# Optimization experiments

Measured on AMD Instinct MI355X. Metric: run time of the kernel, lower is better.

The kernel has to match this reference:

```python
import jax, jax.numpy as jnp
import numpy as np

V, D, M = 13000, 300, 500   # vocab, embed dim, cell/mem size (hardcoded in source)
B, NW, T = 64, 5, 128       # episodes, ways, seq len
EPS = 1e-8                  # torch cosine_similarity default eps


def setup_inputs():
    key = jax.random.key(0)
    ks = jax.random.split(key, 14)
    s = 0.05  # xavier-ish scale
    return {
        "support_tokens": jax.random.randint(ks[0], (B, NW, T), 0, V, dtype=jnp.int32),
        "target_tokens": jax.random.randint(ks[1], (B, T), 0, V, dtype=jnp.int32),
        "blank_pos_support": jax.random.randint(ks[2], (B, NW), 0, T, dtype=jnp.int32),
        "blank_pos_target": jax.random.randint(ks[3], (B,), 0, T, dtype=jnp.int32),
        "target_y": jax.random.randint(ks[4], (B,), 0, NW, dtype=jnp.int32),
        "emb": jax.random.normal(ks[5], (V, D)) * s,
        "WL": jax.random.normal(ks[6], (3, M, D)) * s,
        "UL": jax.random.normal(ks[7], (3, M, M)) * s,
        "bL": jnp.zeros((3, M)),
        "WR": jax.random.normal(ks[8], (3, M, D)) * s,
        "UR": jax.random.normal(ks[9], (3, M, M)) * s,
        "bR": jnp.zeros((3, M)),
        "Wo": jax.random.normal(ks[10], (D, M)) * s,
        "Uo": jax.random.normal(ks[11], (D, M)) * s,
        "bo": jnp.zeros((D,)),
        "c0L": jnp.zeros((M,)),
        "c0R": jnp.zeros((M,)),
    }


def _cell_scan(x, W, U, b, c0):
    # x: [T, D] -> pre-update cell states (the 'env' the source appends BEFORE updating _c): [T, M]
    gx = jnp.einsum('td,gmd->tgm', x, W) + b  # input projections for all 3 gates, all timesteps
    def step(c, g):
        g = g + jnp.einsum('gmh,h->gm', U, c)
        f = jax.nn.sigmoid(g[0])
        i = jax.nn.sigmoid(g[1])
        cbar = jnp.tanh(g[2])
        return f * c + i * cbar, c
    _, pre = jax.lax.scan(step, c0, gx)
    return pre


def _blank_env(tokens, blank_pos, emb, WL, UL, bL, WR, UR, bR, Wo, Uo, bo, c0L, c0R):
    # tokens: [N, T], blank_pos: [N] -> env vector at blank position: [N, D]
    x = emb[tokens]  # [N, T, D]
    Lenv = jax.vmap(lambda xs: _cell_scan(xs, WL, UL, bL, c0L))(x)          # [N, T, M]
    Renv = jax.vmap(lambda xs: _cell_scan(xs[::-1], WR, UR, bR, c0R))(x)[:, ::-1]
    n = jnp.arange(tokens.shape[0])
    l = Lenv[n, blank_pos]  # [N, M]
    r = Renv[n, blank_pos]  # source pairs Lenv[i] with Renv[T-1-i] of the reversed list == right pre-state at pos i
    return jnp.tanh(l @ Wo.T + r @ Uo.T + bo)  # oNN: unbatched_Linear(lev=0, tanh)


def reference(support_tokens, target_tokens, blank_pos_support, blank_pos_target,
              target_y, emb, WL, UL, bL, WR, UR, bR, Wo, Uo, bo, c0L, c0R):
    b, nw, t = support_tokens.shape
    sup = _blank_env(support_tokens.reshape(b * nw, t), blank_pos_support.reshape(b * nw),
                     emb, WL, UL, bL, WR, UR, bR, Wo, Uo, bo, c0L, c0R).reshape(b, nw, -1)
    tgt = _blank_env(target_tokens, blank_pos_target,
                     emb, WL, UL, bL, WR, UR, bR, Wo, Uo, bo, c0L, c0R)  # [B, D]
    # cosine similarity per way, scaled by 10 (fce LSTM output is discarded in the source, so omitted)
    dot = jnp.einsum('bnd,bd->bn', sup, tgt)
    denom = jnp.maximum(jnp.linalg.norm(sup, axis=-1) * jnp.linalg.norm(tgt, axis=-1)[:, None], EPS)
    z = (dot / denom) * 10.0  # [B, NW]
    probs = jax.nn.softmax(z, axis=1)
    accuracy = jnp.mean((jnp.argmax(probs, axis=1) == target_y).astype(jnp.float32))
    # F.cross_entropy applied to the softmax probs (double softmax), as in the source
    logp = jax.nn.log_softmax(probs, axis=1)
    loss = -jnp.mean(jnp.take_along_axis(logp, target_y[:, None].astype(jnp.int32), axis=1))
    return accuracy, loss
```

## Files before the change

### kernel.cpp

```cpp
#include <hip/hip_runtime.h>
#include <math.h>

#define V 13000
#define D 300
#define M 500
#define B 64
#define NW 5
#define T 128
#define NSUP (B*NW)
#define NSEQ (NSUP + B)
#define CT 32
#define NCT 12
#define MT 16
#define KSPL 4
#define CHK 20
#define CKS 10
#define KROW 800
#define NSTEP (T-1)
#define ASTR 68
#define BSTR 36
#define APW (CHK*ASTR)
#define BPW (CHK*BSTR)
#define SMSZ (KSPL*(APW+BPW))
#define NCOMP 768
#define NGATH 12

__device__ __forceinline__ float sigmoidf_(float x){ return 1.0f/(1.0f+expf(-x)); }


__global__ void init_kernel(const float* __restrict__ c0L, const float* __restrict__ c0R,
                            float* __restrict__ actB0, float* __restrict__ c_final)
{
    int idx = blockIdx.x*256 + threadIdx.x;
    if (idx >= 2*M*NSEQ) return;
    int d = idx / (M*NSEQ);
    int rem = idx % (M*NSEQ);
    int m = rem / NSEQ;
    int r = rem % NSEQ;
    float v = d ? c0R[m] : c0L[m];
    actB0[((size_t)d*KROW + 300 + m)*NSEQ + r] = v;
    c_final[((size_t)d*NSEQ + r)*M + m] = v;
}

__global__ void sort_kernel(const int* __restrict__ blank_sup, const int* __restrict__ blank_tgt,
                            int* __restrict__ perm, int* __restrict__ lenR, int* __restrict__ tmax)
{
    __shared__ int L0[NSEQ], L1[NSEQ];
    int tid = threadIdx.x;
    int blank = (tid < NSUP) ? blank_sup[tid] : blank_tgt[tid - NSUP];
    int l0 = blank, l1 = (T-1) - blank;
    L0[tid] = l0; L1[tid] = l1;
    __syncthreads();
    int r0 = 0, r1 = 0;
    for (int j = 0; j < NSEQ; ++j) {
        int c = L0[j]; r0 += (c > l0) || (c == l0 && j < tid);
        int d = L1[j]; r1 += (d > l1) || (d == l1 && j < tid);
    }
    perm[r0] = tid;        lenR[r0] = l0;
    perm[NSEQ + r1] = tid; lenR[NSEQ + r1] = l1;
    __syncthreads();
    if (tid < 2*NCT) {
        int dir = tid / NCT, t = tid % NCT;
        tmax[tid] = lenR[dir*NSEQ + t*CT];
    }
}

__global__ __launch_bounds__(256)
void step_kernel(int s,
                 const float* __restrict__ actB_cur, float* __restrict__ actB_next,
                 float* __restrict__ c_final,
                 const float* __restrict__ WL, const float* __restrict__ UL, const float* __restrict__ bL,
                 const float* __restrict__ WR, const float* __restrict__ UR, const float* __restrict__ bR,
                 const int* __restrict__ perm, const int* __restrict__ lenR, const int* __restrict__ tmax,
                 const int* __restrict__ sup_tok, const int* __restrict__ tgt_tok,
                 const float* __restrict__ emb)
{
    const int bid = blockIdx.x;
    const int tid = threadIdx.x;

    if (bid >= NCOMP) {
        const int gb = bid - NCOMP;
        const int d  = gb / 6;
        const int rt = gb % 6;
        const int sn = s + 1;
        if (sn >= NSTEP) return;
        if (sn >= tmax[d*NCT + 2*rt]) return;
        const int rr = tid & 63;
        const int kk = tid >> 6;
        const int rank = rt*64 + rr;
        const int ch = perm[d*NSEQ + rank];
        const int tpos = d ? (T-1 - sn) : sn;
        const int tok = (ch < NSUP) ? sup_tok[ch*T + tpos] : tgt_tok[(ch-NSUP)*T + tpos];
        const float* src = emb + (size_t)tok*D + kk;
        float* dst = actB_next + (size_t)d*KROW*NSEQ + rank;
        #pragma unroll 5
        for (int k4 = 0; k4 < 75; ++k4) {
            dst[(size_t)(k4*4 + kk)*NSEQ] = src[k4*4];
        }
        return;
    }
    if (s < 0) return;

    const int ct = bid >> 6;
    const int dm = bid & 63;
    const int d  = dm >> 5;
    const int mt = dm & 31;
    if (s >= tmax[d*NCT + ct]) return;

    __shared__ float smem[SMSZ];

    const int ks   = tid >> 6;
    const int lane = tid & 63;
    const int ty   = lane >> 3;
    const int tx   = lane & 7;
    const int rank0 = ct*CT;

    const float* Wd = d ? WR : WL;
    const float* Ud = d ? UR : UL;
    const float* bias = d ? bR : bL;

    float* As = smem + ks*APW;
    float* Bs = smem + KSPL*APW + ks*BPW;

    const float* aW[4]; const float* aU[4]; float* aD[4];
    #pragma unroll
    for (int i = 0; i < 4; ++i) {
        int slot = lane + 64*i; if (slot >= 240) slot = 239;
        int row = slot/5, kq = slot%5;
        int g = row >> 4, ml = row & 15;
        int m = mt*MT + ml; if (m >= M) m = M-1;
        aW[i] = Wd + (size_t)(g*M + m)*D + kq*4;
        aU[i] = Ud + (size_t)(g*M + m)*M + kq*4;
        aD[i] = As + kq*4*ASTR + ml*4 + g;
    }
    const bool a3 = (lane < 48);
    const float* bS[3]; float* bD[3];
    #pragma unroll
    for (int i = 0; i < 3; ++i) {
        int slot = lane + 64*i; if (slot >= 160) slot = 159;
        int kk = slot >> 3, c4 = slot & 7;
        bS[i] = actB_cur + ((size_t)d*KROW + kk)*NSEQ + rank0 + c4*4;
        bD[i] = Bs + kk*BSTR + c4*4;
    }
    const bool b2 = (lane < 32);

    float4 aR4[4]; float4 bR4[3];
    auto loadA = [&](int gc){
        const int off = (gc < 15) ? gc*CHK : gc*CHK - 300;
        const bool isx = (gc < 15);
        aR4[0] = *(const float4*)((isx ? aW[0] : aU[0]) + off);
        aR4[1] = *(const float4*)((isx ? aW[1] : aU[1]) + off);
        aR4[2] = *(const float4*)((isx ? aW[2] : aU[2]) + off);
        if (a3) aR4[3] = *(const float4*)((isx ? aW[3] : aU[3]) + off);
    };
    auto loadB = [&](int gc){
        const size_t ofs = (size_t)(gc*CHK)*NSEQ;
        bR4[0] = *(const float4*)(bS[0] + ofs);
        bR4[1] = *(const float4*)(bS[1] + ofs);
        if (b2) bR4[2] = *(const float4*)(bS[2] + ofs);
    };
    auto writeAB = [&](){
        #pragma unroll
        for (int i = 0; i < 4; ++i) {
            if (i == 3 && !a3) break;
            float* p = aD[i];
            p[0] = aR4[i].x; p[ASTR] = aR4[i].y; p[2*ASTR] = aR4[i].z; p[3*ASTR] = aR4[i].w;
        }
        *(float4*)bD[0] = bR4[0];
        *(float4*)bD[1] = bR4[1];
        if (b2) *(float4*)bD[2] = bR4[2];
    };

    float4 acc[2][3];
    #pragma unroll
    for (int j=0;j<2;++j)
        #pragma unroll
        for (int g=0;g<3;++g) acc[j][g] = make_float4(0.f,0.f,0.f,0.f);

    const float* Ard = As + ty*8;
    const float* Brd = Bs + tx*4;

#define FMA4(AC, AV, BV) AC.x += (AV)*(BV).x; AC.y += (AV)*(BV).y; AC.z += (AV)*(BV).z; AC.w += (AV)*(BV).w;

    loadA(ks*CKS); loadB(ks*CKS);
    for (int ck = 0; ck < CKS; ++ck) {
        writeAB();
        if (ck + 1 < CKS) { loadA(ks*CKS + ck + 1); loadB(ks*CKS + ck + 1); }
        #pragma unroll
        for (int kk = 0; kk < CHK; ++kk) {
            float4 a0 = *(const float4*)(Ard + kk*ASTR);
            float4 a1 = *(const float4*)(Ard + kk*ASTR + 4);
            float4 b  = *(const float4*)(Brd + kk*BSTR);
            FMA4(acc[0][0], a0.x, b);
            FMA4(acc[0][1], a0.y, b);
            FMA4(acc[0][2], a0.z, b);
            FMA4(acc[1][0], a1.x, b);
            FMA4(acc[1][1], a1.y, b);
            FMA4(acc[1][2], a1.z, b);
        }
    }
#undef FMA4

    __syncthreads();
    float* red = smem;
    #pragma unroll
    for (int j=0;j<2;++j) {
        int ml = ty*2 + j;
        #pragma unroll
        for (int g=0;g<3;++g)
            *(float4*)&red[((ks*MT + ml)*3 + g)*CT + tx*4] = acc[j][g];
    }
    __syncthreads();

    #pragma unroll
    for (int q=0;q<2;++q) {
        int cell = tid*2 + q;
        int ml = cell >> 5, c = cell & 31;
        int m = mt*MT + ml;
        if (m < M) {
            float g0 = bias[m], g1 = bias[M + m], g2 = bias[2*M + m];
            #pragma unroll
            for (int kq=0;kq<KSPL;++kq) {
                g0 += red[((kq*MT + ml)*3 + 0)*CT + c];
                g1 += red[((kq*MT + ml)*3 + 1)*CT + c];
                g2 += red[((kq*MT + ml)*3 + 2)*CT + c];
            }
            int rank = rank0 + c;
            int len  = lenR[d*NSEQ + rank];
            size_t cidx = ((size_t)d*KROW + 300 + m)*NSEQ + rank;
            float cold = actB_cur[cidx];
            float f  = sigmoidf_(g0);
            float i2 = sigmoidf_(g1);
            float cb = tanhf(g2);
            float cn = (s < len) ? (f*cold + i2*cb) : cold;
            actB_next[cidx] = cn;
            if (s == len - 1) {
                int ch = perm[d*NSEQ + rank];
                c_final[((size_t)d*NSEQ + ch)*M + m] = cn;
            }
        }
    }
}

__global__ void env_kernel(const float* __restrict__ l_states, const float* __restrict__ r_states,
                           const float* __restrict__ Wo, const float* __restrict__ Uo,
                           const float* __restrict__ bo,
                           float* __restrict__ env)
{
    __shared__ __align__(16) float l[M];
    __shared__ __align__(16) float r[M];
    const int i = blockIdx.x;
    const int tid = threadIdx.x;
    for (int m=tid; m<M; m+=blockDim.x){ l[m]=l_states[i*M+m]; r[m]=r_states[i*M+m]; }
    __syncthreads();
    for (int d=tid; d<D; d+=blockDim.x) {
        const float4* wo = reinterpret_cast<const float4*>(Wo + (size_t)d*M);
        const float4* uo = reinterpret_cast<const float4*>(Uo + (size_t)d*M);
        const float4* lv = reinterpret_cast<const float4*>(l);
        const float4* rv = reinterpret_cast<const float4*>(r);
        float acc = bo[d];
        #pragma unroll 5
        for (int q=0; q<M/4; ++q) {
            float4 a=wo[q], bv=lv[q], u=uo[q], rr=rv[q];
            acc += a.x*bv.x + a.y*bv.y + a.z*bv.z + a.w*bv.w;
            acc += u.x*rr.x + u.y*rr.y + u.z*rr.z + u.w*rr.w;
        }
        env[i*D + d] = tanhf(acc);
    }
}

__global__ void episode_kernel(const float* __restrict__ env, const int* __restrict__ target_y,
                               float* __restrict__ flags, float* __restrict__ losses)
{
    const int b = blockIdx.x;
    const int lane = threadIdx.x;
    const float* tgt = env + (size_t)(NSUP + b)*D;

    float tn = 0.f;
    for (int d=lane; d<D; d+=64){ float v=tgt[d]; tn += v*v; }
    for (int off=32; off; off>>=1) tn += __shfl_down(tn, off);
    tn = __shfl(tn, 0);

    float z[NW];
    for (int n=0; n<NW; ++n){
        const float* sup = env + (size_t)(b*NW + n)*D;
        float dot=0.f, sn=0.f;
        for (int d=lane; d<D; d+=64){ float sv=sup[d], tv=tgt[d]; dot+=sv*tv; sn+=sv*sv; }
        for (int off=32; off; off>>=1){ dot += __shfl_down(dot,off); sn += __shfl_down(sn,off); }
        dot = __shfl(dot,0); sn = __shfl(sn,0);
        float denom = fmaxf(sqrtf(sn)*sqrtf(tn), 1e-8f);
        z[n] = dot/denom*10.0f;
    }

    if (lane==0){
        float mx=z[0];
        for(int n=1;n<NW;n++) mx=fmaxf(mx,z[n]);
        float se=0.f; float p[NW];
        for(int n=0;n<NW;n++){ p[n]=expf(z[n]-mx); se+=p[n]; }
        for(int n=0;n<NW;n++) p[n]/=se;
        int am=0; float bv=p[0];
        for(int n=1;n<NW;n++) if(p[n]>bv){bv=p[n];am=n;}
        int y = target_y[b];
        flags[b] = (am==y)?1.0f:0.0f;
        float mx2=p[0]; for(int n=1;n<NW;n++) mx2=fmaxf(mx2,p[n]);
        float se2=0.f; for(int n=0;n<NW;n++) se2+=expf(p[n]-mx2);
        losses[b] = -(p[y]-mx2-logf(se2));
    }
}

__global__ void finalize_kernel(const float* __restrict__ flags, const float* __restrict__ losses,
                                float* __restrict__ out)
{
    const int lane = threadIdx.x;
    float f = flags[lane], l = losses[lane];
    for (int off=32; off; off>>=1){ f += __shfl_down(f,off); l += __shfl_down(l,off); }
    if (lane==0){ out[0] = f/(float)B; out[1] = l/(float)B; }
}

extern "C" void kernel_launch(void* const* d_in, const int* in_sizes, int n_in,
                              void* d_out, int out_size, void* d_ws, size_t ws_size,
                              hipStream_t stream) {
    const int*   sup_tok   = (const int*)d_in[0];
    const int*   tgt_tok   = (const int*)d_in[1];
    const int*   blank_sup = (const int*)d_in[2];
    const int*   blank_tgt = (const int*)d_in[3];
    const int*   target_y  = (const int*)d_in[4];
    const float* emb = (const float*)d_in[5];
    const float* WL  = (const float*)d_in[6];
    const float* UL  = (const float*)d_in[7];
    const float* bL  = (const float*)d_in[8];
    const float* WR  = (const float*)d_in[9];
    const float* UR  = (const float*)d_in[10];
    const float* bR  = (const float*)d_in[11];
    const float* Wo  = (const float*)d_in[12];
    const float* Uo  = (const float*)d_in[13];
    const float* bo  = (const float*)d_in[14];
    const float* c0L = (const float*)d_in[15];
    const float* c0R = (const float*)d_in[16];

    const size_t ACTSZ = (size_t)2*KROW*NSEQ;
    float* ws_f = (float*)d_ws;
    float* actB0   = ws_f;
    float* actB1   = actB0 + ACTSZ;
    float* c_final = actB1 + ACTSZ;
    float* env     = c_final + 2*NSEQ*M;
    float* flags   = env + NSEQ*D;
    float* losses  = flags + B;
    int*   perm    = (int*)(losses + B);
    int*   lenR    = perm + 2*NSEQ;
    int*   tmax    = lenR + 2*NSEQ;

    init_kernel<<<(2*M*NSEQ + 255)/256, 256, 0, stream>>>(c0L, c0R, actB0, c_final);
    sort_kernel<<<1, NSEQ, 0, stream>>>(blank_sup, blank_tgt, perm, lenR, tmax);

    step_kernel<<<NCOMP + NGATH, 256, 0, stream>>>(-1, actB1, actB0, c_final,
                                                   WL, UL, bL, WR, UR, bR,
                                                   perm, lenR, tmax, sup_tok, tgt_tok, emb);
    for (int s = 0; s < NSTEP; ++s) {
        float* cur  = (s & 1) ? actB1 : actB0;
        float* next = (s & 1) ? actB0 : actB1;
        step_kernel<<<NCOMP + NGATH, 256, 0, stream>>>(s, cur, next, c_final,
                                                       WL, UL, bL, WR, UR, bR,
                                                       perm, lenR, tmax, sup_tok, tgt_tok, emb);
    }

    env_kernel<<<NSEQ, 256, 0, stream>>>(c_final, c_final + NSEQ*M, Wo, Uo, bo, env);
    episode_kernel<<<B, 64, 0, stream>>>(env, target_y, flags, losses);
    finalize_kernel<<<1, 64, 0, stream>>>(flags, losses, (float*)d_out);
}
```

Baseline: 5.100 ms.

## Stream activations from global into registers, keep only weights in LDS

The per-step gate GEMM no longer stages the activation tile through shared memory. Each thread now computes one m-row by three gates by eight columns, reading activation rows straight from global memory through a four-deep register prefetch ring. Only weight rows are written to LDS, in a row-major layout with float4 stores, and the LDS footprint shrinks to what the reduction needs; a launch-bounds occupancy hint of 3 is added. This removes the activation LDS writes and reads, but the 16 lanes sharing a column group now issue duplicate global loads, which depend on L1 broadcast.

```diff
diff --git a/kernel.cpp b/kernel.cpp
--- a/kernel.cpp
+++ b/kernel.cpp
@@ -17,11 +17,9 @@
 #define CKS 10
 #define KROW 800
 #define NSTEP (T-1)
-#define ASTR 68
-#define BSTR 36
-#define APW (CHK*ASTR)
-#define BPW (CHK*BSTR)
-#define SMSZ (KSPL*(APW+BPW))
+#define ASTR 28
+#define APW (48*ASTR)
+#define SMSZ 6144
 #define NCOMP 768
 #define NGATH 12
 
@@ -65,7 +63,7 @@
     }
 }
 
-__global__ __launch_bounds__(256)
+__global__ __launch_bounds__(256, 3)
 void step_kernel(int s,
                  const float* __restrict__ actB_cur, float* __restrict__ actB_next,
                  float* __restrict__ c_final,
@@ -94,9 +92,8 @@
         const float* src = emb + (size_t)tok*D + kk;
         float* dst = actB_next + (size_t)d*KROW*NSEQ + rank;
         #pragma unroll 5
-        for (int k4 = 0; k4 < 75; ++k4) {
+        for (int k4 = 0; k4 < 75; ++k4)
             dst[(size_t)(k4*4 + kk)*NSEQ] = src[k4*4];
-        }
         return;
     }
     if (s < 0) return;
@@ -107,45 +104,36 @@
     const int mt = dm & 31;
     if (s >= tmax[d*NCT + ct]) return;
 
-    __shared__ float smem[SMSZ];
+    __shared__ __align__(16) float smem[SMSZ];
 
     const int ks   = tid >> 6;
     const int lane = tid & 63;
-    const int ty   = lane >> 3;
-    const int tx   = lane & 7;
+    const int ml   = lane >> 2;
+    const int cg   = lane & 3;
     const int rank0 = ct*CT;
+    const int m0 = mt*MT;
 
     const float* Wd = d ? WR : WL;
     const float* Ud = d ? UR : UL;
     const float* bias = d ? bR : bL;
 
     float* As = smem + ks*APW;
-    float* Bs = smem + KSPL*APW + ks*BPW;
 
     const float* aW[4]; const float* aU[4]; float* aD[4];
     #pragma unroll
     for (int i = 0; i < 4; ++i) {
         int slot = lane + 64*i; if (slot >= 240) slot = 239;
         int row = slot/5, kq = slot%5;
-        int g = row >> 4, ml = row & 15;
-        int m = mt*MT + ml; if (m >= M) m = M-1;
+        int g = row >> 4, mr = row & 15;
+        int m = m0 + mr; if (m >= M) m = M-1;
         aW[i] = Wd + (size_t)(g*M + m)*D + kq*4;
         aU[i] = Ud + (size_t)(g*M + m)*M + kq*4;
-        aD[i] = As + kq*4*ASTR + ml*4 + g;
+        aD[i] = As + row*ASTR + kq*4;
     }
     const bool a3 = (lane < 48);
-    const float* bS[3]; float* bD[3];
-    #pragma unroll
-    for (int i = 0; i < 3; ++i) {
-        int slot = lane + 64*i; if (slot >= 160) slot = 159;
-        int kk = slot >> 3, c4 = slot & 7;
-        bS[i] = actB_cur + ((size_t)d*KROW + kk)*NSEQ + rank0 + c4*4;
-        bD[i] = Bs + kk*BSTR + c4*4;
-    }
-    const bool b2 = (lane < 32);
-
-    float4 aR4[4]; float4 bR4[3];
-    auto loadA = [&](int gc){
+
+    float4 aR4[4];
+    auto ldA = [&](int gc){
         const int off = (gc < 15) ? gc*CHK : gc*CHK - 300;
         const bool isx = (gc < 15);
         aR4[0] = *(const float4*)((isx ? aW[0] : aU[0]) + off);
@@ -153,77 +141,84 @@
         aR4[2] = *(const float4*)((isx ? aW[2] : aU[2]) + off);
         if (a3) aR4[3] = *(const float4*)((isx ? aW[3] : aU[3]) + off);
     };
-    auto loadB = [&](int gc){
-        const size_t ofs = (size_t)(gc*CHK)*NSEQ;
-        bR4[0] = *(const float4*)(bS[0] + ofs);
-        bR4[1] = *(const float4*)(bS[1] + ofs);
-        if (b2) bR4[2] = *(const float4*)(bS[2] + ofs);
+    auto wrA = [&](){
+        *(float4*)aD[0] = aR4[0];
+        *(float4*)aD[1] = aR4[1];
+        *(float4*)aD[2] = aR4[2];
+        if (a3) *(float4*)aD[3] = aR4[3];
     };
-    auto writeAB = [&](){
+
+    float4 acc[3][2];
+    #pragma unroll
+    for (int g = 0; g < 3; ++g) { acc[g][0] = make_float4(0.f,0.f,0.f,0.f);
+                                  acc[g][1] = make_float4(0.f,0.f,0.f,0.f); }
+
+    const float* Ard = As + ml*ASTR;
+    const float* bp  = actB_cur + ((size_t)d*KROW + ks*200)*NSEQ + rank0 + cg*8;
+
+    float4 bc[4][2];
+    #pragma unroll
+    for (int q = 0; q < 4; ++q) {
+        bc[q][0] = *(const float4*)(bp + (size_t)q*NSEQ);
+        bc[q][1] = *(const float4*)(bp + (size_t)q*NSEQ + 4);
+    }
+
+#define FMA8(AC, AV, B0, B1) \
+    AC[0].x += (AV)*(B0).x; AC[0].y += (AV)*(B0).y; AC[0].z += (AV)*(B0).z; AC[0].w += (AV)*(B0).w; \
+    AC[1].x += (AV)*(B1).x; AC[1].y += (AV)*(B1).y; AC[1].z += (AV)*(B1).z; AC[1].w += (AV)*(B1).w;
+
+    ldA(ks*CKS);
+    for (int ck = 0; ck < CKS; ++ck) {
+        wrA();
+        if (ck + 1 < CKS) ldA(ks*CKS + ck + 1);
         #pragma unroll
-        for (int i = 0; i < 4; ++i) {
-            if (i == 3 && !a3) break;
-            float* p = aD[i];
-            p[0] = aR4[i].x; p[ASTR] = aR4[i].y; p[2*ASTR] = aR4[i].z; p[3*ASTR] = aR4[i].w;
+        for (int t2 = 0; t2 < 10; ++t2) {
+            const int kk = t2*2;
+            float2 a0 = *(const float2*)(Ard + kk);
+            float2 a1 = *(const float2*)(Ard + 16*ASTR + kk);
+            float2 a2 = *(const float2*)(Ard + 32*ASTR + kk);
+            #pragma unroll
+            for (int sub = 0; sub < 2; ++sub) {
+                const int tt = kk + sub;
+                const int rg = tt & 3;
+                float ax0 = sub ? a0.y : a0.x;
+                float ax1 = sub ? a1.y : a1.x;
+                float ax2 = sub ? a2.y : a2.x;
+                float4 b0 = bc[rg][0], b1 = bc[rg][1];
+                int gt = ck*CHK + tt;
+                if (gt + 4 < 200) {
+                    bc[rg][0] = *(const float4*)(bp + (size_t)(gt+4)*NSEQ);
+                    bc[rg][1] = *(const float4*)(bp + (size_t)(gt+4)*NSEQ + 4);
+                }
+                FMA8(acc[0], ax0, b0, b1);
+                FMA8(acc[1], ax1, b0, b1);
+                FMA8(acc[2], ax2, b0, b1);
+            }
         }
-        *(float4*)bD[0] = bR4[0];
-        *(float4*)bD[1] = bR4[1];
-        if (b2) *(float4*)bD[2] = bR4[2];
-    };
-
-    float4 acc[2][3];
-    #pragma unroll
-    for (int j=0;j<2;++j)
-        #pragma unroll
-        for (int g=0;g<3;++g) acc[j][g] = make_float4(0.f,0.f,0.f,0.f);
-
-    const float* Ard = As + ty*8;
-    const float* Brd = Bs + tx*4;
-
-#define FMA4(AC, AV, BV) AC.x += (AV)*(BV).x; AC.y += (AV)*(BV).y; AC.z += (AV)*(BV).z; AC.w += (AV)*(BV).w;
-
-    loadA(ks*CKS); loadB(ks*CKS);
-    for (int ck = 0; ck < CKS; ++ck) {
-        writeAB();
-        if (ck + 1 < CKS) { loadA(ks*CKS + ck + 1); loadB(ks*CKS + ck + 1); }
-        #pragma unroll
-        for (int kk = 0; kk < CHK; ++kk) {
-            float4 a0 = *(const float4*)(Ard + kk*ASTR);
-            float4 a1 = *(const float4*)(Ard + kk*ASTR + 4);
-            float4 b  = *(const float4*)(Brd + kk*BSTR);
-            FMA4(acc[0][0], a0.x, b);
-            FMA4(acc[0][1], a0.y, b);
-            FMA4(acc[0][2], a0.z, b);
-            FMA4(acc[1][0], a1.x, b);
-            FMA4(acc[1][1], a1.y, b);
-            FMA4(acc[1][2], a1.z, b);
-        }
-    }
-#undef FMA4
+    }
+#undef FMA8
 
     __syncthreads();
     float* red = smem;
     #pragma unroll
-    for (int j=0;j<2;++j) {
-        int ml = ty*2 + j;
-        #pragma unroll
-        for (int g=0;g<3;++g)
-            *(float4*)&red[((ks*MT + ml)*3 + g)*CT + tx*4] = acc[j][g];
-    }
-    __syncthreads();
-
-    #pragma unroll
-    for (int q=0;q<2;++q) {
+    for (int g = 0; g < 3; ++g) {
+        *(float4*)&red[((ks*MT + ml)*3 + g)*CT + cg*8]     = acc[g][0];
+        *(float4*)&red[((ks*MT + ml)*3 + g)*CT + cg*8 + 4] = acc[g][1];
+    }
+    __syncthreads();
+
+    #pragma unroll
+    for (int q = 0; q < 2; ++q) {
         int cell = tid*2 + q;
-        int ml = cell >> 5, c = cell & 31;
-        int m = mt*MT + ml;
+        int mr = cell >> 5, c = cell & 31;
+        int m = m0 + mr;
         if (m < M) {
             float g0 = bias[m], g1 = bias[M + m], g2 = bias[2*M + m];
             #pragma unroll
-            for (int kq=0;kq<KSPL;++kq) {
-                g0 += red[((kq*MT + ml)*3 + 0)*CT + c];
-                g1 += red[((kq*MT + ml)*3 + 1)*CT + c];
-                g2 += red[((kq*MT + ml)*3 + 2)*CT + c];
+            for (int kq = 0; kq < KSPL; ++kq) {
+                g0 += red[((kq*MT + mr)*3 + 0)*CT + c];
+                g1 += red[((kq*MT + mr)*3 + 1)*CT + c];
+                g2 += red[((kq*MT + mr)*3 + 2)*CT + c];
             }
             int rank = rank0 + c;
             int len  = lenR[d*NSEQ + rank];
```

Result: slower. 6.473 ms (+26.9%).
